# Optimization experiments

Hardware: AMD Instinct MI355X
Metric: run time of the kernel (lower is better)

Reference implementation:

```python
import jax, jax.numpy as jnp
import numpy as np

B, T, D, H = 2, 2048, 1024, 16
HD = D // H  # 64
SCALE = 1.0 / np.sqrt(D).astype(np.float32)  # module uses 1/sqrt(mod_dim), not head_dim


def setup_inputs() -> dict:
    key = jax.random.key(0)
    k1, k2, k3 = jax.random.split(key, 3)
    x = jax.random.normal(k1, (B, T, D), dtype=jnp.float32)
    W_attn = jax.random.normal(k2, (3 * D, D), dtype=jnp.float32) * 0.02
    W_out = jax.random.normal(k3, (D, D), dtype=jnp.float32) * 0.02
    return {"x": x, "W_attn": W_attn, "W_out": W_out}


def reference(x, W_attn, W_out):
    b, t, d = x.shape
    # qkv projection (Linear, no bias): x @ W^T
    qkv = jnp.einsum('btd,ed->bte', x, W_attn)  # [b, t, 3d]
    q, k, v = jnp.split(qkv, 3, axis=-1)
    # [b, h, t, hd]
    q = q.reshape(b, t, H, HD).transpose(0, 2, 1, 3)
    k = k.reshape(b, t, H, HD).transpose(0, 2, 1, 3)
    v = v.reshape(b, t, H, HD).transpose(0, 2, 1, 3)
    # raw scores, causal mask applied before scaling (scale*-inf == -inf, so
    # equivalent to the original mask-then-scale order)
    att = jnp.einsum('bhqd,bhkd->bhqk', q, k)
    causal = jnp.tril(jnp.ones((t, t), dtype=bool))
    att = jnp.where(causal[None, None], att * SCALE, -jnp.inf)
    att = jax.nn.softmax(att, axis=-1)
    z = jnp.einsum('bhqk,bhkd->bhqd', att, v)
    z = z.transpose(0, 2, 1, 3).reshape(b, t, d)
    return jnp.einsum('btd,od->bto', z, W_out)
```

## Files before the change

kernel.cpp:

```cpp
#include <hip/hip_runtime.h>
#include <cstddef>

typedef unsigned short u16;
typedef __attribute__((ext_vector_type(4))) float floatx4;
typedef __attribute__((ext_vector_type(8))) short short8;
typedef __attribute__((ext_vector_type(4))) unsigned int uintx4;

#define TT 2048
#define DD 1024
#define NH 16
#define ATT_SCALE (1.0f / 32.0f)

__device__ __forceinline__ u16 f2bf(float f) {
  unsigned u = __builtin_bit_cast(unsigned, f);
  u += 0x7fffu + ((u >> 16) & 1u);
  return (u16)(u >> 16);
}

__device__ __forceinline__ unsigned pack2(float a, float b) {
#if __has_builtin(__builtin_amdgcn_cvt_pk_bf16_f32)
  auto t = __builtin_amdgcn_cvt_pk_bf16_f32(a, b);
  return __builtin_bit_cast(unsigned, t);
#else
  unsigned ua = __builtin_bit_cast(unsigned, a);
  ua += 0x7fffu + ((ua >> 16) & 1u);
  unsigned ub = __builtin_bit_cast(unsigned, b);
  ub += 0x7fffu + ((ub >> 16) & 1u);
  return (ua >> 16) | (ub & 0xffff0000u);
#endif
}

__device__ __forceinline__ void g2l16(const u16* g, u16* l) {
#if __has_builtin(__builtin_amdgcn_global_load_lds)
  __builtin_amdgcn_global_load_lds(
      (const __attribute__((address_space(1))) unsigned int*)g,
      (__attribute__((address_space(3))) unsigned int*)l, 16, 0, 0);
#else
  *(int4*)l = *(const int4*)g;
#endif
}

__device__ __forceinline__ short8 scale_q(short8 q) {
  short8 r;
#pragma unroll
  for (int i = 0; i < 8; ++i) {
    float f = __builtin_bit_cast(float, ((unsigned)(u16)q[i]) << 16) * ATT_SCALE;
    r[i] = (short)f2bf(f);
  }
  return r;
}

__global__ __launch_bounds__(256) void cvt3_kernel(const float* __restrict__ a,
                                                   const float* __restrict__ b,
                                                   const float* __restrict__ c,
                                                   u16* __restrict__ out,
                                                   int na, int nb, int nc) {
  int i = blockIdx.x * 256 + threadIdx.x;
  const float* src;
  int j;
  if (i < na) { src = a; j = i; }
  else if (i < na + nb) { src = b; j = i - na; }
  else if (i < na + nb + nc) { src = c; j = i - na - nb; }
  else return;
  float4 v = ((const float4*)src)[j];
  ((ushort4*)out)[i] = make_ushort4(f2bf(v.x), f2bf(v.y), f2bf(v.z), f2bf(v.w));
}

template <int MODE, int BN>
__global__ __launch_bounds__(256) void gemm_ep(const u16* __restrict__ A,
                                               const u16* __restrict__ Bm,
                                               void* __restrict__ C,
                                               u16* __restrict__ vt,
                                               int M, int N, int K) {
  constexpr int NT = BN / 32;
  __shared__ __attribute__((aligned(16))) unsigned char shmem[32768];
  u16* As = (u16*)shmem;
  u16* Bs = As + 2 * 128 * 32;

  const int tid = threadIdx.x;
  const int lane = tid & 63;
  const int wave = tid >> 6;
  const int quad = lane >> 4;
  const int l16 = lane & 15;
  const int wm = (wave >> 1) * 64;
  const int wn = (wave & 1) * (BN / 2);
  const int m0 = blockIdx.x * 128;
  const int n0 = blockIdx.y * BN;

  const int srow = tid >> 2;
  const int scol = (tid & 3) * 8;
  const int sl = tid * 8;

  floatx4 acc[4][NT] = {};

  auto stage = [&](int b, int k0) {
    g2l16(&A[(size_t)(m0 + srow) * K + k0 + scol], &As[b * 4096 + sl]);
    g2l16(&A[(size_t)(m0 + 64 + srow) * K + k0 + scol], &As[b * 4096 + 2048 + sl]);
    g2l16(&Bm[(size_t)(n0 + srow) * K + k0 + scol], &Bs[b * (BN * 32) + sl]);
    if (BN == 128)
      g2l16(&Bm[(size_t)(n0 + 64 + srow) * K + k0 + scol], &Bs[b * 4096 + 2048 + sl]);
  };
  auto compute = [&](int b) {
    short8 af[4];
#pragma unroll
    for (int mt = 0; mt < 4; ++mt)
      af[mt] = *(const short8*)&As[b * 4096 + (wm + mt * 16 + l16) * 32 + quad * 8];
#pragma unroll
    for (int nt = 0; nt < NT; ++nt) {
      short8 bf = *(const short8*)&Bs[b * (BN * 32) + (wn + nt * 16 + l16) * 32 + quad * 8];
#pragma unroll
      for (int mt = 0; mt < 4; ++mt)
        acc[mt][nt] = __builtin_amdgcn_mfma_f32_16x16x32_bf16(af[mt], bf, acc[mt][nt], 0, 0, 0);
    }
  };

  stage(0, 0);
  for (int k0 = 0; k0 < K; k0 += 64) {
    __syncthreads();
    if (k0 + 32 < K) stage(1, k0 + 32);
    compute(0);
    __syncthreads();
    if (k0 + 64 < K) stage(0, k0 + 64);
    compute(1);
  }

  __syncthreads();

  if (MODE == 2 && n0 >= 2048) {
    u16* scr = (u16*)shmem;
    const int bidx = m0 >> 11;
    const int tb = m0 & 2047;
#pragma unroll
    for (int mt = 0; mt < 4; ++mt)
#pragma unroll
      for (int nt = 0; nt < NT; ++nt) {
        int nl = wn + nt * 16 + l16;
        int tl = wm + mt * 16 + quad * 4;
        int sz = (nl & 7) << 3;
        *(unsigned*)&scr[nl * 128 + (tl ^ sz)] = pack2(acc[mt][nt][0], acc[mt][nt][1]);
        *(unsigned*)&scr[nl * 128 + ((tl + 2) ^ sz)] = pack2(acc[mt][nt][2], acc[mt][nt][3]);
      }
    __syncthreads();
#pragma unroll
    for (int ps = 0; ps < 8; ++ps) {
      int nl = ps * 16 + (tid >> 4);
      int ck = (tid & 15) * 8;
      int sz = (nl & 7) << 3;
      int4 v = *(const int4*)&scr[nl * 128 + (ck ^ sz)];
      size_t vrow = (size_t)(bidx * 1024 + n0 + nl - 2048);
      *(int4*)&vt[vrow * TT + tb + ck] = v;
    }
  } else if (MODE >= 1) {
    const int cw = (MODE == 2) ? 2048 : N;
    constexpr int SH = (BN == 128) ? 5 : 4;
    u16* scr = (u16*)shmem;
#pragma unroll
    for (int mt = 0; mt < 4; ++mt)
#pragma unroll
      for (int nt = 0; nt < NT; ++nt)
#pragma unroll
        for (int r = 0; r < 4; ++r) {
          int ml = wm + mt * 16 + quad * 4 + r;
          int nl = wn + nt * 16 + l16;
          scr[ml * BN + (nl ^ (((ml >> 2) & 3) << SH))] = f2bf(acc[mt][nt][r]);
        }
    __syncthreads();
    constexpr int RPP = 2048 / BN;
    constexpr int CPT = BN / 8;
#pragma unroll
    for (int ps = 0; ps < 128 / RPP; ++ps) {
      int ml = ps * RPP + tid / CPT;
      int ck = (tid % CPT) * 8;
      int sz = ((ml >> 2) & 3) << SH;
      int4 v = *(const int4*)&scr[ml * BN + (ck ^ sz)];
      *(int4*)&((u16*)C)[(size_t)(m0 + ml) * cw + n0 + ck] = v;
    }
  } else {
    float* scrf = (float*)shmem;
#pragma unroll
    for (int mt = 0; mt < 4; ++mt)
#pragma unroll
      for (int nt = 0; nt < NT; ++nt)
#pragma unroll
        for (int r = 0; r < 4; ++r) {
          int ml = wm + mt * 16 + quad * 4 + r;
          int nl = wn + nt * 16 + l16;
          scrf[ml * 64 + (nl ^ (((ml >> 2) & 3) << 4))] = acc[mt][nt][r];
        }
    __syncthreads();
#pragma unroll
    for (int ps = 0; ps < 8; ++ps) {
      int ml = ps * 16 + (tid >> 4);
      int ck = (tid & 15) * 4;
      int sz = ((ml >> 2) & 3) << 4;
      float4 v = *(const float4*)&scrf[ml * 64 + (ck ^ sz)];
      *(float4*)&((float*)C)[(size_t)(m0 + ml) * N + n0 + ck] = v;
    }
  }
}

template <bool DIAG>
__device__ __forceinline__ void exp_pack(const floatx4* s, int kt0, int quad,
                                         int qr, float& ps, unsigned W[4][2]) {
#pragma unroll
  for (int nt = 0; nt < 4; ++nt) {
    float e[4];
#pragma unroll
    for (int r = 0; r < 4; ++r) {
      float v = __expf(s[nt][r]);
      if (DIAG) {
        int kk = kt0 + nt * 16 + quad * 4 + r;
        v = (kk <= qr) ? v : 0.f;
      }
      ps += v;
      e[r] = v;
    }
    W[nt][0] = pack2(e[0], e[1]);
    W[nt][1] = pack2(e[2], e[3]);
  }
}

__device__ __forceinline__ void pfrag(const unsigned W[4][2], int bpA, int bpB,
                                      int quad, short8& pa0, short8& pa1) {
  uintx4 a, b;
#pragma unroll
  for (int c = 0; c < 2; ++c) {
    unsigned x0 = (unsigned)__builtin_amdgcn_ds_bpermute(bpA, (int)W[0][c]);
    unsigned x1 = (unsigned)__builtin_amdgcn_ds_bpermute(bpA, (int)W[1][c]);
    unsigned y0 = (unsigned)__builtin_amdgcn_ds_bpermute(bpB, (int)W[0][c]);
    unsigned y1 = (unsigned)__builtin_amdgcn_ds_bpermute(bpB, (int)W[1][c]);
    a[c]     = (quad < 2) ? x0 : x1;
    a[2 + c] = (quad < 2) ? y0 : y1;
    unsigned u0 = (unsigned)__builtin_amdgcn_ds_bpermute(bpA, (int)W[2][c]);
    unsigned u1 = (unsigned)__builtin_amdgcn_ds_bpermute(bpA, (int)W[3][c]);
    unsigned t0 = (unsigned)__builtin_amdgcn_ds_bpermute(bpB, (int)W[2][c]);
    unsigned t1 = (unsigned)__builtin_amdgcn_ds_bpermute(bpB, (int)W[3][c]);
    b[c]     = (quad < 2) ? u0 : u1;
    b[2 + c] = (quad < 2) ? t0 : t1;
  }
  pa0 = __builtin_bit_cast(short8, a);
  pa1 = __builtin_bit_cast(short8, b);
}

__global__ __launch_bounds__(512, 4) void attn_flash8(const u16* __restrict__ qk,
                                                      const u16* __restrict__ vt,
                                                      u16* __restrict__ z) {
  __shared__ u16 Ks[2][64 * 64];
  __shared__ u16 Vs[2][64 * 64];

  const int tid = threadIdx.x;
  const int lane = tid & 63;
  const int wave = tid >> 6;
  const int qs = wave & 3;
  const int par = wave >> 2;
  const int quad = lane >> 4;
  const int l16 = lane & 15;

  const int p = blockIdx.x;
  const int qtA = p, qtB = 31 - p;
  const int bh = blockIdx.y;
  const int b = bh >> 4, h = bh & 15;

  const size_t bbase = (size_t)b * TT * 2048;
  const u16* qg = qk + bbase + h * 64;
  const u16* kg = qk + bbase + 1024 + h * 64;
  const u16* vtg = vt + (size_t)bh * 64 * TT;

  short8 qfA[2], qfB[2];
  {
    const size_t ra = (size_t)(qtA * 64 + qs * 16 + l16) * 2048;
    const size_t rb = (size_t)(qtB * 64 + qs * 16 + l16) * 2048;
    qfA[0] = scale_q(*(const short8*)&qg[ra + quad * 8]);
    qfA[1] = scale_q(*(const short8*)&qg[ra + 32 + quad * 8]);
    qfB[0] = scale_q(*(const short8*)&qg[rb + quad * 8]);
    qfB[1] = scale_q(*(const short8*)&qg[rb + 32 + quad * 8]);
  }

  floatx4 OA[4] = {}, OB[4] = {};
  float psA = 0.f, psB = 0.f;

  const int tsel = tid >> 8;
  const int t8 = tid & 255;
  const int str = t8 >> 2, sc = (t8 & 3) * 16;
  const int swr = (str & 7) << 3;

  const int nktB = qtB + 1;
  const int M = (nktB + 1) >> 1;
  const int qrA = qtA * 64 + qs * 16 + l16;
  const int qrB = qtB * 64 + qs * 16 + l16;

  const int sw = (l16 & 7) << 3;
  const int rc0 = (quad * 8) ^ sw;
  const int rc1 = (32 + quad * 8) ^ sw;
  const int bpA = ((((lane >> 4) & 1) << 5) | l16) << 2;
  const int bpB = bpA + 64;

  int4 kr0, kr1, vr0, vr1;
  {
    const size_t kro = (size_t)(tsel * 64 + str) * 2048 + sc;
    const size_t vro = (size_t)str * TT + tsel * 64 + sc;
    kr0 = *(const int4*)&kg[kro];
    kr1 = *(const int4*)&kg[kro + 8];
    vr0 = *(const int4*)&vtg[vro];
    vr1 = *(const int4*)&vtg[vro + 8];
  }

  for (int m = 0; m < M; ++m) {
    const int kt = 2 * m + par;
    const int kt0 = kt * 64;
    __syncthreads();
    if (2 * m + tsel < nktB) {
      *(int4*)&Ks[tsel][str * 64 + (sc ^ swr)] = kr0;
      *(int4*)&Ks[tsel][str * 64 + ((sc + 8) ^ swr)] = kr1;
      *(int4*)&Vs[tsel][str * 64 + (sc ^ swr)] = vr0;
      *(int4*)&Vs[tsel][str * 64 + ((sc + 8) ^ swr)] = vr1;
    }
    __syncthreads();
    {
      const int kst = 2 * (m + 1) + tsel;
      if (kst < nktB) {
        const size_t kro = (size_t)(kst * 64 + str) * 2048 + sc;
        const size_t vro = (size_t)str * TT + kst * 64 + sc;
        kr0 = *(const int4*)&kg[kro];
        kr1 = *(const int4*)&kg[kro + 8];
        vr0 = *(const int4*)&vtg[vro];
        vr1 = *(const int4*)&vtg[vro + 8];
      }
    }

    if (kt < nktB) {
      floatx4 s[4];
      __builtin_amdgcn_s_setprio(1);
#pragma unroll
      for (int nt = 0; nt < 4; ++nt) {
        const int ro = (nt * 16 + l16) * 64;
        short8 k0 = *(const short8*)&Ks[par][ro + rc0];
        short8 k1 = *(const short8*)&Ks[par][ro + rc1];
        floatx4 zz = {0.f, 0.f, 0.f, 0.f};
        s[nt] = __builtin_amdgcn_mfma_f32_16x16x32_bf16(k0, qfB[0], zz, 0, 0, 0);
        s[nt] = __builtin_amdgcn_mfma_f32_16x16x32_bf16(k1, qfB[1], s[nt], 0, 0, 0);
      }
      __builtin_amdgcn_s_setprio(0);
      short8 pa0, pa1;
      {
        unsigned W[4][2];
        if (kt == qtB)
          exp_pack<true>(s, kt0, quad, qrB, psB, W);
        else
          exp_pack<false>(s, kt0, quad, qrB, psB, W);
        pfrag(W, bpA, bpB, quad, pa0, pa1);
      }
      __builtin_amdgcn_s_setprio(1);
#pragma unroll
      for (int nt = 0; nt < 4; ++nt) {
        const int ro = (nt * 16 + l16) * 64;
        short8 v0 = *(const short8*)&Vs[par][ro + rc0];
        short8 v1 = *(const short8*)&Vs[par][ro + rc1];
        OB[nt] = __builtin_amdgcn_mfma_f32_16x16x32_bf16(pa0, v0, OB[nt], 0, 0, 0);
        OB[nt] = __builtin_amdgcn_mfma_f32_16x16x32_bf16(pa1, v1, OB[nt], 0, 0, 0);
      }
      __builtin_amdgcn_s_setprio(0);

      if (kt <= qtA) {
        __builtin_amdgcn_s_setprio(1);
#pragma unroll
        for (int nt = 0; nt < 4; ++nt) {
          const int ro = (nt * 16 + l16) * 64;
          short8 k0 = *(const short8*)&Ks[par][ro + rc0];
          short8 k1 = *(const short8*)&Ks[par][ro + rc1];
          floatx4 zz = {0.f, 0.f, 0.f, 0.f};
          s[nt] = __builtin_amdgcn_mfma_f32_16x16x32_bf16(k0, qfA[0], zz, 0, 0, 0);
          s[nt] = __builtin_amdgcn_mfma_f32_16x16x32_bf16(k1, qfA[1], s[nt], 0, 0, 0);
        }
        __builtin_amdgcn_s_setprio(0);
        {
          unsigned W[4][2];
          if (kt == qtA)
            exp_pack<true>(s, kt0, quad, qrA, psA, W);
          else
            exp_pack<false>(s, kt0, quad, qrA, psA, W);
          pfrag(W, bpA, bpB, quad, pa0, pa1);
        }
        __builtin_amdgcn_s_setprio(1);
#pragma unroll
        for (int nt = 0; nt < 4; ++nt) {
          const int ro = (nt * 16 + l16) * 64;
          short8 v0 = *(const short8*)&Vs[par][ro + rc0];
          short8 v1 = *(const short8*)&Vs[par][ro + rc1];
          OA[nt] = __builtin_amdgcn_mfma_f32_16x16x32_bf16(pa0, v0, OA[nt], 0, 0, 0);
          OA[nt] = __builtin_amdgcn_mfma_f32_16x16x32_bf16(pa1, v1, OA[nt], 0, 0, 0);
        }
        __builtin_amdgcn_s_setprio(0);
      }
    }
  }

  psA += __shfl_xor(psA, 16);
  psA += __shfl_xor(psA, 32);
  psB += __shfl_xor(psB, 16);
  psB += __shfl_xor(psB, 32);

  float* red = (float*)Ks;
  float* lred = (float*)Vs;

  __syncthreads();
  if (par == 1) {
#pragma unroll
    for (int nt = 0; nt < 4; ++nt)
#pragma unroll
      for (int r = 0; r < 4; ++r)
        red[(qs * 16 + quad * 4 + r) * 64 + nt * 16 + l16] = OA[nt][r];
  }
  if (quad == 0) lred[par * 64 + qs * 16 + l16] = psA;
  __syncthreads();
  if (par == 0) {
#pragma unroll
    for (int r = 0; r < 4; ++r) {
      int row = qs * 16 + quad * 4 + r;
      float rl = 1.0f / (lred[row] + lred[64 + row]);
      int qa = qtA * 64 + row;
#pragma unroll
      for (int nt = 0; nt < 4; ++nt) {
        float o = OA[nt][r] + red[row * 64 + nt * 16 + l16];
        z[(size_t)(b * TT + qa) * DD + h * 64 + nt * 16 + l16] = f2bf(o * rl);
      }
    }
  }
  __syncthreads();
  if (par == 1) {
#pragma unroll
    for (int nt = 0; nt < 4; ++nt)
#pragma unroll
      for (int r = 0; r < 4; ++r)
        red[(qs * 16 + quad * 4 + r) * 64 + nt * 16 + l16] = OB[nt][r];
  }
  if (quad == 0) lred[par * 64 + qs * 16 + l16] = psB;
  __syncthreads();
  if (par == 0) {
#pragma unroll
    for (int r = 0; r < 4; ++r) {
      int row = qs * 16 + quad * 4 + r;
      float rl = 1.0f / (lred[row] + lred[64 + row]);
      int qb = qtB * 64 + row;
#pragma unroll
      for (int nt = 0; nt < 4; ++nt) {
        float o = OB[nt][r] + red[row * 64 + nt * 16 + l16];
        z[(size_t)(b * TT + qb) * DD + h * 64 + nt * 16 + l16] = f2bf(o * rl);
      }
    }
  }
}

extern "C" void kernel_launch(void* const* d_in, const int* in_sizes, int n_in,
                              void* d_out, int out_size, void* d_ws, size_t ws_size,
                              hipStream_t stream) {
  const float* x  = (const float*)d_in[0];
  const float* Wa = (const float*)d_in[1];
  const float* Wo = (const float*)d_in[2];
  float* out = (float*)d_out;

  u16* xb  = (u16*)d_ws;
  u16* Wab = xb  + (size_t)4096 * 1024;
  u16* Wob = Wab + (size_t)3072 * 1024;
  u16* qk  = Wob + (size_t)1024 * 1024;
  u16* z   = qk  + (size_t)4096 * 2048;
  u16* vt  = z   + (size_t)4096 * 1024;

  cvt3_kernel<<<8192, 256, 0, stream>>>(x, Wa, Wo, xb, 1048576, 786432, 262144);

  gemm_ep<2, 128><<<dim3(32, 24), 256, 0, stream>>>(xb, Wab, qk, vt, 4096, 3072, 1024);

  attn_flash8<<<dim3(16, 2 * NH), 512, 0, stream>>>(qk, vt, z);

  gemm_ep<0, 64><<<dim3(32, 16), 256, 0, stream>>>(z, Wob, out, nullptr, 4096, 1024, 1024);
}
```

Baseline: 168.0 us.

## Replace QKV projection GEMM with 256x256-tile, 512-thread double-buffered kernel

Adds a dedicated QKV projection kernel that uses 256x256 output tiles, 8 waves, direct global-to-LDS double buffering with explicit vmcnt waits and barriers, and raised wave priority around the MFMA block. The larger tiles raise arithmetic intensity per LDS load and reduce global traffic relative to the previous 128x128 tile GEMM. The V-transpose epilogue moves into the new kernel and the old MODE 2 path is trimmed. The grid shrinks to 192 blocks on a large-CU device and uses 128KB of LDS per block, so occupancy and load balance may suffer.

```diff
diff --git a/kernel.cpp b/kernel.cpp
--- a/kernel.cpp
+++ b/kernel.cpp
@@ -66,6 +66,129 @@
   ((ushort4*)out)[i] = make_ushort4(f2bf(v.x), f2bf(v.y), f2bf(v.z), f2bf(v.w));
 }
 
+__global__ __launch_bounds__(512, 2) void gemm256_qkv(const u16* __restrict__ A,
+                                                      const u16* __restrict__ Bm,
+                                                      u16* __restrict__ qk,
+                                                      u16* __restrict__ vt) {
+  constexpr int K = 1024;
+  __shared__ u16 sh[4 * 16384];
+  u16* As0 = sh;
+  u16* As1 = sh + 16384;
+  u16* Bs0 = sh + 32768;
+  u16* Bs1 = sh + 49152;
+
+  const int tid = threadIdx.x;
+  const int lane = tid & 63;
+  const int wave = tid >> 6;
+  const int quad = lane >> 4;
+  const int l16 = lane & 15;
+  const int wm = (wave >> 2) * 128;
+  const int wn = (wave & 3) * 64;
+  const int m0 = blockIdx.x * 256;
+  const int n0 = blockIdx.y * 256;
+
+  const int srow = tid >> 3;
+  const int scol = ((tid & 7) ^ (srow & 7)) * 8;
+  const int sdst = tid * 8;
+  const int sw = l16 & 7;
+
+  floatx4 acc[8][4] = {};
+
+  auto stage = [&](u16* Ad, u16* Bd, int k0) {
+#pragma unroll
+    for (int o = 0; o < 4; ++o)
+      g2l16(&A[(size_t)(m0 + o * 64 + srow) * K + k0 + scol], &Ad[o * 4096 + sdst]);
+#pragma unroll
+    for (int o = 0; o < 4; ++o)
+      g2l16(&Bm[(size_t)(n0 + o * 64 + srow) * K + k0 + scol], &Bd[o * 4096 + sdst]);
+  };
+
+  auto compute = [&](const u16* Ab, const u16* Bb) {
+    short8 bf[4][2];
+#pragma unroll
+    for (int nt = 0; nt < 4; ++nt) {
+      const int rn = (wn + nt * 16 + l16) * 64;
+#pragma unroll
+      for (int kk = 0; kk < 2; ++kk)
+        bf[nt][kk] = *(const short8*)&Bb[rn + ((((kk << 2) | quad) ^ sw) * 8)];
+    }
+    __builtin_amdgcn_s_setprio(1);
+#pragma unroll
+    for (int mt = 0; mt < 8; ++mt) {
+      const int rm = (wm + mt * 16 + l16) * 64;
+      short8 a0 = *(const short8*)&Ab[rm + ((quad ^ sw) * 8)];
+      short8 a1 = *(const short8*)&Ab[rm + (((4 | quad) ^ sw) * 8)];
+#pragma unroll
+      for (int nt = 0; nt < 4; ++nt) {
+        acc[mt][nt] = __builtin_amdgcn_mfma_f32_16x16x32_bf16(a0, bf[nt][0], acc[mt][nt], 0, 0, 0);
+        acc[mt][nt] = __builtin_amdgcn_mfma_f32_16x16x32_bf16(a1, bf[nt][1], acc[mt][nt], 0, 0, 0);
+      }
+    }
+    __builtin_amdgcn_s_setprio(0);
+  };
+
+  stage(As0, Bs0, 0);
+  for (int kt = 0; kt < 16; kt += 2) {
+    stage(As1, Bs1, (kt + 1) << 6);
+    asm volatile("s_waitcnt vmcnt(8)\ns_barrier" ::: "memory");
+    compute(As0, Bs0);
+    asm volatile("s_barrier" ::: "memory");
+    if (kt < 14) {
+      stage(As0, Bs0, (kt + 2) << 6);
+      asm volatile("s_waitcnt vmcnt(8)\ns_barrier" ::: "memory");
+    } else {
+      asm volatile("s_waitcnt vmcnt(0)\ns_barrier" ::: "memory");
+    }
+    compute(As1, Bs1);
+    asm volatile("s_barrier" ::: "memory");
+  }
+
+  u16* scr = sh;
+  if (n0 >= 2048) {
+    const int bidx = m0 >> 11;
+    const int tb = m0 & 2047;
+#pragma unroll
+    for (int mt = 0; mt < 8; ++mt)
+#pragma unroll
+      for (int nt = 0; nt < 4; ++nt) {
+        int nl = wn + nt * 16 + l16;
+        int tl = wm + mt * 16 + quad * 4;
+        int swz = (nl & 7) << 3;
+        *(unsigned*)&scr[nl * 256 + (tl ^ swz)] = pack2(acc[mt][nt][0], acc[mt][nt][1]);
+        *(unsigned*)&scr[nl * 256 + ((tl + 2) ^ swz)] = pack2(acc[mt][nt][2], acc[mt][nt][3]);
+      }
+    __syncthreads();
+#pragma unroll
+    for (int ps = 0; ps < 16; ++ps) {
+      int nl = ps * 16 + (tid >> 5);
+      int c = tid & 31;
+      int4 v = *(const int4*)&scr[nl * 256 + ((c ^ (nl & 7)) * 8)];
+      size_t vrow = (size_t)(bidx * 1024 + n0 - 2048 + nl);
+      *(int4*)&vt[vrow * TT + tb + c * 8] = v;
+    }
+  } else {
+#pragma unroll
+    for (int mt = 0; mt < 8; ++mt)
+#pragma unroll
+      for (int nt = 0; nt < 4; ++nt)
+#pragma unroll
+        for (int r = 0; r < 4; ++r) {
+          int ml = wm + mt * 16 + quad * 4 + r;
+          int nl = wn + nt * 16 + l16;
+          scr[ml * 256 + (nl ^ (((ml >> 2) & 3) << 4))] = f2bf(acc[mt][nt][r]);
+        }
+    __syncthreads();
+#pragma unroll
+    for (int ps = 0; ps < 16; ++ps) {
+      int ml = ps * 16 + (tid >> 5);
+      int c = tid & 31;
+      int cc = c ^ (((ml >> 2) & 3) << 1);
+      int4 v = *(const int4*)&scr[ml * 256 + cc * 8];
+      *(int4*)&qk[(size_t)(m0 + ml) * 2048 + n0 + c * 8] = v;
+    }
+  }
+}
+
 template <int MODE, int BN>
 __global__ __launch_bounds__(256) void gemm_ep(const u16* __restrict__ A,
                                                const u16* __restrict__ Bm,
@@ -126,32 +249,8 @@
 
   __syncthreads();
 
-  if (MODE == 2 && n0 >= 2048) {
-    u16* scr = (u16*)shmem;
-    const int bidx = m0 >> 11;
-    const int tb = m0 & 2047;
-#pragma unroll
-    for (int mt = 0; mt < 4; ++mt)
-#pragma unroll
-      for (int nt = 0; nt < NT; ++nt) {
-        int nl = wn + nt * 16 + l16;
-        int tl = wm + mt * 16 + quad * 4;
-        int sz = (nl & 7) << 3;
-        *(unsigned*)&scr[nl * 128 + (tl ^ sz)] = pack2(acc[mt][nt][0], acc[mt][nt][1]);
-        *(unsigned*)&scr[nl * 128 + ((tl + 2) ^ sz)] = pack2(acc[mt][nt][2], acc[mt][nt][3]);
-      }
-    __syncthreads();
-#pragma unroll
-    for (int ps = 0; ps < 8; ++ps) {
-      int nl = ps * 16 + (tid >> 4);
-      int ck = (tid & 15) * 8;
-      int sz = (nl & 7) << 3;
-      int4 v = *(const int4*)&scr[nl * 128 + (ck ^ sz)];
-      size_t vrow = (size_t)(bidx * 1024 + n0 + nl - 2048);
-      *(int4*)&vt[vrow * TT + tb + ck] = v;
-    }
-  } else if (MODE >= 1) {
-    const int cw = (MODE == 2) ? 2048 : N;
+  if (MODE >= 1) {
+    const int cw = N;
     constexpr int SH = (BN == 128) ? 5 : 4;
     u16* scr = (u16*)shmem;
 #pragma unroll
@@ -468,7 +567,7 @@
 
   cvt3_kernel<<<8192, 256, 0, stream>>>(x, Wa, Wo, xb, 1048576, 786432, 262144);
 
-  gemm_ep<2, 128><<<dim3(32, 24), 256, 0, stream>>>(xb, Wab, qk, vt, 4096, 3072, 1024);
+  gemm256_qkv<<<dim3(16, 12), 512, 0, stream>>>(xb, Wab, qk, vt);
 
   attn_flash8<<<dim3(16, 2 * NH), 512, 0, stream>>>(qk, vt, z);
 
```

Result: no change. 169.2 us (+0.7%).
